# Kernel optimization log

Measured on AMD Instinct MI355X. Metric: run time of the kernel, lower is better.

The kernel has to match this reference:

```python
import jax, jax.numpy as jnp
import numpy as np


def _interpn_linear(vol, loc):
    """Trilinear interpolation matching voxelmorph/neuron interpn.
    vol: [X, Y, Z, C]; loc: [X, Y, Z, 3] absolute sample coordinates.
    """
    spatial = vol.shape[:-1]
    ndims = len(spatial)
    max_f = jnp.asarray([d - 1 for d in spatial], dtype=loc.dtype)
    max_i = jnp.asarray([d - 1 for d in spatial], dtype=jnp.int32)

    loc = jnp.clip(loc, 0.0, max_f)          # clipped_loc
    loc0 = jnp.floor(loc)
    loc0i = jnp.clip(loc0.astype(jnp.int32), 0, max_i)
    loc1i = jnp.clip(loc0i + 1, 0, max_i)

    # voxelmorph weights: corner-0 weight = loc1 - clipped_loc, corner-1 = 1 - that
    w_lo = loc1i.astype(loc.dtype) - loc      # weight for taking loc0
    w_hi = 1.0 - w_lo                          # weight for taking loc1

    out = jnp.zeros(vol.shape, vol.dtype)
    for c in range(2 ** ndims):
        bits = [(c >> d) & 1 for d in range(ndims)]
        idx = tuple(jnp.where(bits[d], loc1i[..., d], loc0i[..., d]) if False else (loc1i[..., d] if bits[d] else loc0i[..., d]) for d in range(ndims))
        w = jnp.ones(loc.shape[:-1], loc.dtype)
        for d in range(ndims):
            w = w * (w_hi[..., d] if bits[d] else w_lo[..., d])
        out = out + vol[idx] * w[..., None]
    return out


def setup_inputs() -> dict:
    key = jax.random.key(0)
    k1, k2 = jax.random.split(key)
    vol = jax.random.normal(k1, (2, 160, 160, 160, 1), dtype=jnp.float32)
    flow = jax.random.normal(k2, (2, 160, 160, 160, 3), dtype=jnp.float32)
    return {"vol": vol, "flow": flow}


def reference(vol, flow):
    # dense displacement field: absolute location = identity grid + flow
    spatial = vol.shape[1:-1]
    grid = jnp.stack(
        jnp.meshgrid(*[jnp.arange(d, dtype=flow.dtype) for d in spatial], indexing="ij"),
        axis=-1,
    )  # [X,Y,Z,3]
    loc = grid[None] + flow  # [B,X,Y,Z,3]
    return jax.vmap(_interpn_linear)(vol, loc)
```

## Files before the change

kernel.cpp:

```cpp
#include <hip/hip_runtime.h>


#define DIM 160
#define DD  (DIM * DIM)
#define DDD (DIM * DIM * DIM)
#define BATCH 2
#define TOTAL (BATCH * DDD)

__global__ __launch_bounds__(256) void st_warp_kernel(
    const float* __restrict__ vol,
    const float* __restrict__ flow,
    float* __restrict__ out)
{
    int idx = blockIdx.x * blockDim.x + threadIdx.x;
    if (idx >= TOTAL) return;

    int b   = idx / DDD;
    int rem = idx - b * DDD;
    int x   = rem / DD;
    int r2  = rem - x * DD;
    int y   = r2 / DIM;
    int z   = r2 - y * DIM;

    const float* f = flow + (size_t)idx * 3;
    float fx = f[0];
    float fy = f[1];
    float fz = f[2];

    const float maxf = (float)(DIM - 1);

    float lx = fminf(fmaxf((float)x + fx, 0.0f), maxf);
    float ly = fminf(fmaxf((float)y + fy, 0.0f), maxf);
    float lz = fminf(fmaxf((float)z + fz, 0.0f), maxf);

    int x0 = (int)floorf(lx);
    int y0 = (int)floorf(ly);
    int z0 = (int)floorf(lz);
    x0 = min(max(x0, 0), DIM - 1);
    y0 = min(max(y0, 0), DIM - 1);
    z0 = min(max(z0, 0), DIM - 1);

    int x1 = min(x0 + 1, DIM - 1);
    int y1 = min(y0 + 1, DIM - 1);
    int z1 = min(z0 + 1, DIM - 1);

    float wx0 = (float)x1 - lx;  float wx1 = 1.0f - wx0;
    float wy0 = (float)y1 - ly;  float wy1 = 1.0f - wy0;
    float wz0 = (float)z1 - lz;  float wz1 = 1.0f - wz0;

    const float* vb = vol + (size_t)b * DDD;

    int bx0 = x0 * DD, bx1 = x1 * DD;
    int by0 = y0 * DIM, by1 = y1 * DIM;

    float v000 = vb[bx0 + by0 + z0];
    float v100 = vb[bx1 + by0 + z0];
    float v010 = vb[bx0 + by1 + z0];
    float v110 = vb[bx1 + by1 + z0];
    float v001 = vb[bx0 + by0 + z1];
    float v101 = vb[bx1 + by0 + z1];
    float v011 = vb[bx0 + by1 + z1];
    float v111 = vb[bx1 + by1 + z1];

    float acc;
    acc  = v000 * (wx0 * wy0 * wz0);
    acc += v100 * (wx1 * wy0 * wz0);
    acc += v010 * (wx0 * wy1 * wz0);
    acc += v110 * (wx1 * wy1 * wz0);
    acc += v001 * (wx0 * wy0 * wz1);
    acc += v101 * (wx1 * wy0 * wz1);
    acc += v011 * (wx0 * wy1 * wz1);
    acc += v111 * (wx1 * wy1 * wz1);

    out[idx] = acc;
}

extern "C" void kernel_launch(void* const* d_in, const int* in_sizes, int n_in,
                              void* d_out, int out_size, void* d_ws, size_t ws_size,
                              hipStream_t stream)
{
    const float* vol  = (const float*)d_in[0];
    const float* flow = (const float*)d_in[1];
    float* out = (float*)d_out;

    int blocks = (TOTAL + 255) / 256;
    st_warp_kernel<<<blocks, 256, 0, stream>>>(vol, flow, out);
}
```

Measured before the change: 226.3 us.

## Stage flow through LDS with vector loads, swizzle blocks per XCD, nontemporal I/O

Each block now loads its 256x3 flow values with coalesced 16-byte nontemporal loads into shared memory, replacing the strided 3-float per-thread global reads. Block IDs are remapped so each XCD handles a contiguous chunk of the volume, which is meant to improve L2 locality for the gathered vol reads. Output stores are nontemporal to avoid polluting cache. The changes add a __syncthreads, drop the bounds check, and depend on TOTAL dividing evenly into 256-element blocks and 8 XCDs.

```diff
diff --git a/kernel.cpp b/kernel.cpp
--- a/kernel.cpp
+++ b/kernel.cpp
@@ -1,19 +1,38 @@
 #include <hip/hip_runtime.h>
 
+
+typedef float f32x4 __attribute__((ext_vector_type(4)));
 
 #define DIM 160
 #define DD  (DIM * DIM)
 #define DDD (DIM * DIM * DIM)
 #define BATCH 2
 #define TOTAL (BATCH * DDD)
+#define BLK 256
+#define NBLK (TOTAL / BLK)
+#define NXCD 8
+#define CHUNK (NBLK / NXCD)
 
 __global__ __launch_bounds__(256) void st_warp_kernel(
     const float* __restrict__ vol,
     const float* __restrict__ flow,
     float* __restrict__ out)
 {
-    int idx = blockIdx.x * blockDim.x + threadIdx.x;
-    if (idx >= TOTAL) return;
+    __shared__ float sflow[BLK * 3];
+
+    int tid = threadIdx.x;
+    int bid = blockIdx.x;
+    int swz  = (bid & 7) * CHUNK + (bid >> 3);
+    int base = swz * BLK;
+
+    const f32x4* fsrc = (const f32x4*)(flow + (size_t)base * 3);
+    if (tid < 192) {
+        f32x4 v = __builtin_nontemporal_load(&fsrc[tid]);
+        ((f32x4*)sflow)[tid] = v;
+    }
+    __syncthreads();
+
+    int idx = base + tid;
 
     int b   = idx / DDD;
     int rem = idx - b * DDD;
@@ -22,10 +41,9 @@
     int y   = r2 / DIM;
     int z   = r2 - y * DIM;
 
-    const float* f = flow + (size_t)idx * 3;
-    float fx = f[0];
-    float fy = f[1];
-    float fz = f[2];
+    float fx = sflow[tid * 3 + 0];
+    float fy = sflow[tid * 3 + 1];
+    float fz = sflow[tid * 3 + 2];
 
     const float maxf = (float)(DIM - 1);
 
@@ -72,7 +90,7 @@
     acc += v011 * (wx0 * wy1 * wz1);
     acc += v111 * (wx1 * wy1 * wz1);
 
-    out[idx] = acc;
+    __builtin_nontemporal_store(acc, &out[idx]);
 }
 
 extern "C" void kernel_launch(void* const* d_in, const int* in_sizes, int n_in,
@@ -83,6 +101,5 @@
     const float* flow = (const float*)d_in[1];
     float* out = (float*)d_out;
 
-    int blocks = (TOTAL + 255) / 256;
-    st_warp_kernel<<<blocks, 256, 0, stream>>>(vol, flow, out);
+    st_warp_kernel<<<NBLK, BLK, 0, stream>>>(vol, flow, out);
 }
```

Result: no change. 226.9 us (+0.3%).
